# Performance work log

Hardware: AMD Instinct MI355X
Metric: run time of the kernel (lower is better)

Reference implementation:

```python
import jax, jax.numpy as jnp
import numpy as np

S, W, H = 1025, 128, 200


def setup_inputs() -> dict:
    key = jax.random.key(0)
    ks = jax.random.split(key, 40)
    n = lambda k, shape, s=1.0: jax.random.normal(k, shape, dtype=jnp.float32) * s
    p = {}
    p["words"] = n(ks[0], (S, W, H))
    p["lengths"] = jax.random.randint(ks[1], (S,), 1, W + 1, dtype=jnp.int32)
    p["h0w"] = n(ks[2], (S, H))
    p["c0w"] = n(ks[3], (S, H))
    p["h0p"] = n(ks[4], (H,))
    p["c0p"] = n(ks[5], (H,))
    p["h0q"] = n(ks[6], (H,))
    p["c0q"] = n(ks[7], (H,))
    ki = 8
    for nm in ("ctx", "tgt", "prev", "post"):
        p[f"wih_{nm}"] = n(ks[ki], (4 * H, H), 0.05); ki += 1
        p[f"whh_{nm}"] = n(ks[ki], (4 * H, H), 0.05); ki += 1
        p[f"bih_{nm}"] = n(ks[ki], (4 * H,), 0.05); ki += 1
        p[f"bhh_{nm}"] = n(ks[ki], (4 * H,), 0.05); ki += 1
    p["fc_w"] = n(ks[ki], (H, 2 * H), 0.05); ki += 1
    p["fc_b"] = n(ks[ki], (H,), 0.05)
    return p


def _lstm_seq(x, h0, c0, wih, whh, bih, bhh):
    """x: [T,H]; returns outputs [T,H]. Torch LSTM gate order: i,f,g,o."""
    gx = x @ wih.T + (bih + bhh)  # precompute input projection: [T,4H]
    def step(carry, g):
        h, c = carry
        gates = g + h @ whh.T
        i, f, gg, o = jnp.split(gates, 4, axis=-1)
        c = jax.nn.sigmoid(f) * c + jax.nn.sigmoid(i) * jnp.tanh(gg)
        h = jax.nn.sigmoid(o) * jnp.tanh(c)
        return (h, c), h
    _, hs = jax.lax.scan(step, (h0, c0), gx)
    return hs


def reference(words, lengths, h0w, c0w, h0p, c0p, h0q, c0q,
              wih_ctx, whh_ctx, bih_ctx, bhh_ctx,
              wih_tgt, whh_tgt, bih_tgt, bhh_tgt,
              wih_prev, whh_prev, bih_prev, bhh_prev,
              wih_post, whh_post, bih_post, bhh_post,
              fc_w, fc_b):
    Sn = words.shape[0]
    mid = (Sn - 1) // 2
    # Word-level context RNN over all sentences (batched scan)
    ctx_outs = jax.vmap(_lstm_seq, in_axes=(0, 0, 0, None, None, None, None))(
        words, h0w, c0w, wih_ctx, whh_ctx, bih_ctx, bhh_ctx)  # [S,W,H]
    # sentence embedding = output at last real word (ragged lengths)
    emb = ctx_outs[jnp.arange(Sn), lengths - 1]  # [S,H]
    # middle sentence uses target RNN instead
    tgt_outs = _lstm_seq(words[mid], h0w[mid], c0w[mid], wih_tgt, whh_tgt, bih_tgt, bhh_tgt)
    emb = emb.at[mid].set(tgt_outs[lengths[mid] - 1])
    # prev RNN over sentences 0..mid; keep output at mid
    prev_hs = _lstm_seq(emb[:mid + 1], h0p, c0p, wih_prev, whh_prev, bih_prev, bhh_prev)
    prev_out = prev_hs[-1]
    # post RNN over sentences S-1..mid (reversed); keep output at mid
    post_hs = _lstm_seq(emb[mid:][::-1], h0q, c0q, wih_post, whh_post, bih_post, bhh_post)
    post_out = post_hs[-1]
    feat = jnp.concatenate([prev_out, post_out])  # [2H]
    return feat @ fc_w.T + fc_b  # [H]
```

## Files before the change

### kernel.cpp

```cpp
#include <hip/hip_runtime.h>
#include <cmath>

typedef unsigned short u16;
typedef short bf16x8 __attribute__((ext_vector_type(8)));
typedef float f32x4 __attribute__((ext_vector_type(4)));

#define S_N 1025
#define W_N 128
#define H_N 200
#define FH_N 800
#define KP 232
#define SGP 911
#define SGW 900
#define MID 512
#define NT 56
#define PKT (NT * 7 * 512)

__device__ __forceinline__ float bf2f(u16 u) {
  unsigned int x = ((unsigned int)u) << 16;
  return __builtin_bit_cast(float, x);
}
__device__ __forceinline__ u16 f2bf(float f) {
  unsigned int x = __builtin_bit_cast(unsigned int, f);
  x += 0x7fffu + ((x >> 16) & 1u);
  return (u16)(x >> 16);
}
#define LOG2E 1.44269504088896f
__device__ __forceinline__ float fsigm(float x) {
  float e = __builtin_amdgcn_exp2f(-fabsf(x) * LOG2E);
  float p = __builtin_amdgcn_rcpf(1.f + e);
  return x >= 0.f ? p : 1.f - p;
}
__device__ __forceinline__ float ftanh(float x) {
  float e = __builtin_amdgcn_exp2f(-2.f * fabsf(x) * LOG2E);
  float th = (1.f - e) * __builtin_amdgcn_rcpf(1.f + e);
  return x >= 0.f ? th : -th;
}

__device__ __forceinline__ const bf16x8* pkptr(const u16* pk, int tt, int kcc, int lane) {
  return (const bf16x8*)(pk + (size_t)((tt * 7 + kcc) * 512 + lane * 8));
}

__device__ __forceinline__ int bfidx(int m, int k) {
  return (k >> 5) * 512 + ((((k >> 3) & 3) * 16 + m) << 3) + (k & 7);
}

__global__ __launch_bounds__(256) void k_w2b(
    const float* __restrict__ p0, const float* __restrict__ p1,
    const float* __restrict__ p2, const float* __restrict__ p3,
    const float* __restrict__ p4, const float* __restrict__ p5,
    const float* __restrict__ p6, const float* __restrict__ p7,
    u16* __restrict__ dst)
{
  int i = blockIdx.x * 256 + threadIdx.x;
  if (i >= 8 * PKT) return;
  int w = i / PKT, r = i - w * PKT;
  int tt = r / 3584;
  int q = r - tt * 3584;
  int kcc = q >> 9;
  int lane = (q >> 3) & 63;
  int j = q & 7;
  int col = lane & 15, quad = lane >> 4;
  int gate = tt * 16 + col;
  int k = kcc * 32 + quad * 8 + j;
  const float* ps[8] = {p0, p1, p2, p3, p4, p5, p6, p7};
  u16 v = 0;
  if (gate < FH_N && k < H_N) v = f2bf(ps[w][(size_t)gate * H_N + k]);
  dst[i] = v;
}

__global__ __launch_bounds__(1024) void k_sort(
    const int* __restrict__ lengths, int* __restrict__ order)
{
  __shared__ int key[2048], val[2048];
  int tid = threadIdx.x;
  for (int v = 0; v < 2; ++v) {
    int i = tid + v * 1024;
    key[i] = (i < S_N) ? lengths[i] : -1;
    val[i] = (i < S_N) ? i : (S_N - 1);
  }
  __syncthreads();
  for (int k = 2; k <= 2048; k <<= 1)
    for (int j = k >> 1; j > 0; j >>= 1) {
      for (int v = 0; v < 2; ++v) {
        int i = tid + v * 1024;
        int ix = i ^ j;
        if (ix > i) {
          bool descRegion = ((i & k) == 0);
          int ki = key[i], kx = key[ix];
          if ((ki < kx) == descRegion) {
            key[i] = kx; key[ix] = ki;
            int tv = val[i]; val[i] = val[ix]; val[ix] = tv;
          }
        }
      }
      __syncthreads();
    }
  for (int v = 0; v < 2; ++v) {
    int i = tid + v * 1024;
    if (i < S_N) order[i] = val[i];
  }
}

__global__ __launch_bounds__(512, 1) void k_xpack(
    int c, int CH,
    const float* __restrict__ words, const int* __restrict__ lengths,
    const u16* __restrict__ wihb_ctx, const float* __restrict__ bih_ctx, const float* __restrict__ bhh_ctx,
    const u16* __restrict__ wihb_tgt, const float* __restrict__ bih_tgt, const float* __restrict__ bhh_tgt,
    float* __restrict__ gxc)
{
  const int slot = blockIdx.x % 1026;
  const int tile = blockIdx.x / 1026;
  const int t0f = tile * 16;
  const bool tg = (slot == 1025);
  const int s = tg ? MID : slot;
  const int len = lengths[s];
  const int tbase = c * CH + t0f;
  if (t0f >= CH || tbase >= len) return;
  const u16* wih = tg ? wihb_tgt : wihb_ctx;
  const float* bih = tg ? bih_tgt : bih_ctx;
  const float* bhh = tg ? bhh_tgt : bhh_ctx;

  __shared__ __align__(16) u16 sXh[7 * 512];
  __shared__ __align__(16) u16 sXl[7 * 512];
  __shared__ float sBias[FH_N];
  const int tid = threadIdx.x;
  for (int e = tid; e < 7 * 512; e += 512) { sXh[e] = 0; sXl[e] = 0; }
  for (int e = tid; e < FH_N; e += 512) sBias[e] = bih[e] + bhh[e];
  __syncthreads();
  const int nrow = min(16, min(CH - t0f, len - tbase));
  for (int e = tid; e < nrow * H_N; e += 512) {
    int tr = e / H_N, k = e - tr * H_N;
    float v = words[((size_t)s * W_N + tbase + tr) * H_N + k];
    u16 vh = f2bf(v);
    int idx = bfidx(tr, k);
    sXh[idx] = vh;
    sXl[idx] = f2bf(v - bf2f(vh));
  }
  __syncthreads();

  const int lane = tid & 63, wv = tid >> 6, quad = lane >> 4, col = lane & 15;
  f32x4 acc[7];
#pragma unroll
  for (int i = 0; i < 7; ++i) { f32x4 z = {0.f, 0.f, 0.f, 0.f}; acc[i] = z; }

#pragma unroll
  for (int kcc = 0; kcc < 7; ++kcc) {
    bf16x8 Aw[7];
#pragma unroll
    for (int i = 0; i < 7; ++i) Aw[i] = *pkptr(wih, wv + 8 * i, kcc, lane);
    bf16x8 bxh = *(const bf16x8*)(sXh + kcc * 512 + lane * 8);
    bf16x8 bxl = *(const bf16x8*)(sXl + kcc * 512 + lane * 8);
#pragma unroll
    for (int i = 0; i < 7; ++i) {
      acc[i] = __builtin_amdgcn_mfma_f32_16x16x32_bf16(Aw[i], bxh, acc[i], 0, 0, 0);
      acc[i] = __builtin_amdgcn_mfma_f32_16x16x32_bf16(Aw[i], bxl, acc[i], 0, 0, 0);
    }
  }

  const int tcg = t0f + col;
  const bool okcol = (tcg < CH) && (c * CH + tcg < len);
#pragma unroll
  for (int i = 0; i < 7; ++i) {
    int tt = wv + 8 * i;
    if (tt < 50 && okcol) {
      float bias0 = sBias[tt * 16 + quad * 4 + 0];
      float bias1 = sBias[tt * 16 + quad * 4 + 1];
      float bias2 = sBias[tt * 16 + quad * 4 + 2];
      float bias3 = sBias[tt * 16 + quad * 4 + 3];
      f32x4 o = {acc[i][0] + bias0, acc[i][1] + bias1, acc[i][2] + bias2, acc[i][3] + bias3};
      *(f32x4*)(gxc + ((size_t)slot * CH + tcg) * FH_N + tt * 16 + quad * 4) = o;
    }
  }
}

__global__ __launch_bounds__(512, 1) void k_wrec(
    int c, int CH,
    const int* __restrict__ lengths, const int* __restrict__ order,
    const float* __restrict__ h0w, const float* __restrict__ c0w,
    const u16* __restrict__ whhb_ctx, const u16* __restrict__ whhb_tgt,
    const float* __restrict__ gxc,
    float* __restrict__ stateH, float* __restrict__ stateC,
    float* __restrict__ emb)
{
  const int tid = threadIdx.x;
  const int b = blockIdx.x;
  const bool is_tgt = (b == 65);
  const u16* whh = is_tgt ? whhb_tgt : whhb_ctx;

  __shared__ __align__(16) u16 sBh[7 * 512];
  __shared__ __align__(16) u16 sBl[7 * 512];
  __shared__ float sG[16 * SGW];
  __shared__ int sLen[16], sId[16];

  if (tid < 16) {
    int slot = b * 16 + tid;
    int s = is_tgt ? MID : order[min(slot, S_N - 1)];
    sId[tid] = s;
    sLen[tid] = lengths[s];
  }
  __syncthreads();
  int Lmax = 1;
  for (int m = 0; m < 16; ++m) Lmax = max(Lmax, sLen[m]);
  if (c * CH >= Lmax) return;

  const int lane = tid & 63;
  const int wv = tid >> 6;
  const int quad = lane >> 4;
  const int col = lane & 15;

  bf16x8 afr[7][7];
#pragma unroll
  for (int i = 0; i < 7; ++i)
#pragma unroll
    for (int kcc = 0; kcc < 7; ++kcc)
      afr[i][kcc] = *pkptr(whh, wv + 8 * i, kcc, lane);

  for (int e = tid; e < 7 * 512; e += 512) { sBh[e] = 0; sBl[e] = 0; }
  __syncthreads();

  float creg[7];
#pragma unroll
  for (int rr = 0; rr < 7; ++rr) {
    int e = tid + 512 * rr;
    if (e < 16 * H_N) {
      int m = e / H_N, j = e - m * H_N;
      float h, cc;
      if (c == 0) {
        int s = sId[m];
        h = h0w[(size_t)s * H_N + j];
        cc = c0w[(size_t)s * H_N + j];
      } else {
        h = stateH[(size_t)(b * 16 + m) * H_N + j];
        cc = stateC[(size_t)(b * 16 + m) * H_N + j];
      }
      creg[rr] = cc;
      u16 hh = f2bf(h);
      int idx = bfidx(m, j);
      sBh[idx] = hh;
      sBl[idx] = f2bf(h - bf2f(hh));
    }
  }
  __syncthreads();

#pragma unroll 1
  for (int tc = 0; tc < CH; ++tc) {
    const int t = c * CH + tc;
    if (t >= Lmax) break;

    f32x4 acc[7];
#pragma unroll
    for (int i = 0; i < 7; ++i) { f32x4 z = {0.f, 0.f, 0.f, 0.f}; acc[i] = z; }
#pragma unroll
    for (int kcc = 0; kcc < 7; ++kcc) {
      bf16x8 bh = *(const bf16x8*)(sBh + kcc * 512 + lane * 8);
      bf16x8 bl = *(const bf16x8*)(sBl + kcc * 512 + lane * 8);
#pragma unroll
      for (int i = 0; i < 7; ++i) {
        acc[i] = __builtin_amdgcn_mfma_f32_16x16x32_bf16(afr[i][kcc], bh, acc[i], 0, 0, 0);
        acc[i] = __builtin_amdgcn_mfma_f32_16x16x32_bf16(afr[i][kcc], bl, acc[i], 0, 0, 0);
      }
    }
#pragma unroll
    for (int i = 0; i < 7; ++i) {
      int tt = wv + 8 * i;
      *(f32x4*)(sG + col * SGW + tt * 16 + quad * 4) = acc[i];
    }
    __syncthreads();

#pragma unroll
    for (int rr = 0; rr < 7; ++rr) {
      int e = tid + 512 * rr;
      if (e < 16 * H_N) {
        int m = e / H_N, j = e - m * H_N;
        int gslot = is_tgt ? 1025 : sId[m];
        const float* gp = gxc + ((size_t)gslot * CH + tc) * FH_N + j;
        const float* gRow = sG + m * SGW + j;
        float ig = gRow[0] + gp[0];
        float fg = gRow[H_N] + gp[H_N];
        float gg = gRow[2 * H_N] + gp[2 * H_N];
        float og = gRow[3 * H_N] + gp[3 * H_N];
        float nc = fsigm(fg) * creg[rr] + fsigm(ig) * ftanh(gg);
        float nh = fsigm(og) * ftanh(nc);
        creg[rr] = nc;
        u16 hh = f2bf(nh);
        int idx = bfidx(m, j);
        sBh[idx] = hh;
        sBl[idx] = f2bf(nh - bf2f(hh));
        if (t == sLen[m] - 1) {
          int s = sId[m];
          if (is_tgt) {
            if (m == 0) emb[(size_t)MID * H_N + j] = nh;
          } else if (s != MID) {
            emb[(size_t)s * H_N + j] = nh;
          }
        }
      }
    }
    __syncthreads();
  }

#pragma unroll
  for (int rr = 0; rr < 7; ++rr) {
    int e = tid + 512 * rr;
    if (e < 16 * H_N) {
      int m = e / H_N, j = e - m * H_N;
      int idx = bfidx(m, j);
      stateH[(size_t)(b * 16 + m) * H_N + j] = bf2f(sBh[idx]) + bf2f(sBl[idx]);
      stateC[(size_t)(b * 16 + m) * H_N + j] = creg[rr];
    }
  }
}

__global__ __launch_bounds__(512, 1) void k_word_s(
    const float* __restrict__ words, const int* __restrict__ lengths,
    const int* __restrict__ order,
    const float* __restrict__ h0w, const float* __restrict__ c0w,
    const u16* __restrict__ wihb_ctx, const u16* __restrict__ whhb_ctx,
    const float* __restrict__ bih_ctx, const float* __restrict__ bhh_ctx,
    const u16* __restrict__ wihb_tgt, const u16* __restrict__ whhb_tgt,
    const float* __restrict__ bih_tgt, const float* __restrict__ bhh_tgt,
    float* __restrict__ emb)
{
  const int tid = threadIdx.x;
  const int b = blockIdx.x;
  const bool is_tgt = (b == 65);
  const u16* wih = is_tgt ? wihb_tgt : wihb_ctx;
  const u16* whh = is_tgt ? whhb_tgt : whhb_ctx;
  const float* bih = is_tgt ? bih_tgt : bih_ctx;
  const float* bhh = is_tgt ? bhh_tgt : bhh_ctx;

  __shared__ __align__(16) u16 sXhi[16 * KP];
  __shared__ __align__(16) u16 sXlo[16 * KP];
  __shared__ __align__(16) u16 sHi[16 * KP];
  __shared__ __align__(16) u16 sLo[16 * KP];
  __shared__ float sG[8 * SGP];
  __shared__ float sB[4 * H_N];
  __shared__ int sLen[16], sId[16];

  for (int e = tid; e < 16 * KP; e += 512) {
    sXhi[e] = 0; sXlo[e] = 0; sHi[e] = 0; sLo[e] = 0;
  }
  if (tid < 16) {
    int slot = b * 16 + tid;
    int s = is_tgt ? MID : order[min(slot, S_N - 1)];
    sId[tid] = s;
    sLen[tid] = lengths[s];
  }
  for (int e = tid; e < 4 * H_N; e += 512) sB[e] = bih[e] + bhh[e];
  __syncthreads();

  float creg[7];
#pragma unroll
  for (int r = 0; r < 7; ++r) {
    int e = tid + 512 * r;
    if (e < 16 * H_N) {
      int m = e / H_N, j = e - m * H_N;
      int s = sId[m];
      float h = h0w[(size_t)s * H_N + j];
      u16 hh = f2bf(h);
      sHi[m * KP + j] = hh;
      sLo[m * KP + j] = f2bf(h - bf2f(hh));
      creg[r] = c0w[(size_t)s * H_N + j];
    }
  }
  __syncthreads();
  int Lmax = 1;
  for (int m = 0; m < 16; ++m) Lmax = max(Lmax, sLen[m]);

  const int lane = tid & 63;
  const int wv = tid >> 6;
  const int quad = lane >> 4;
  const int col = lane & 15;
  const int hpass = quad >> 1;

  const u16* aXh = sXhi + col * KP + quad * 8;
  const u16* aXl = sXlo + col * KP + quad * 8;
  const u16* aHh = sHi  + col * KP + quad * 8;
  const u16* aHl = sLo  + col * KP + quad * 8;

#pragma unroll 1
  for (int t = 0; t < Lmax; ++t) {
    for (int e = tid; e < 16 * H_N; e += 512) {
      int m = e / H_N, k = e - m * H_N;
      float v = words[((size_t)sId[m] * W_N + t) * H_N + k];
      u16 vh = f2bf(v);
      sXhi[m * KP + k] = vh;
      sXlo[m * KP + k] = f2bf(v - bf2f(vh));
    }
    __syncthreads();

    f32x4 acc[7];
#pragma unroll
    for (int i = 0; i < 7; ++i) { f32x4 z4 = {0.f, 0.f, 0.f, 0.f}; acc[i] = z4; }

#pragma unroll
    for (int kcc = 0; kcc < 7; ++kcc) {
      bf16x8 axh = *(const bf16x8*)(aXh + kcc * 32);
      bf16x8 axl = *(const bf16x8*)(aXl + kcc * 32);
      bf16x8 ahh = *(const bf16x8*)(aHh + kcc * 32);
      bf16x8 ahl = *(const bf16x8*)(aHl + kcc * 32);
#pragma unroll
      for (int i = 0; i < 7; ++i) {
        bf16x8 bw = *pkptr(wih, wv + 8 * i, kcc, lane);
        bf16x8 bh = *pkptr(whh, wv + 8 * i, kcc, lane);
        acc[i] = __builtin_amdgcn_mfma_f32_16x16x32_bf16(axh, bw, acc[i], 0, 0, 0);
        acc[i] = __builtin_amdgcn_mfma_f32_16x16x32_bf16(axl, bw, acc[i], 0, 0, 0);
        acc[i] = __builtin_amdgcn_mfma_f32_16x16x32_bf16(ahh, bh, acc[i], 0, 0, 0);
        acc[i] = __builtin_amdgcn_mfma_f32_16x16x32_bf16(ahl, bh, acc[i], 0, 0, 0);
      }
    }

#pragma unroll 1
    for (int h = 0; h < 2; ++h) {
      if (hpass == h) {
#pragma unroll
        for (int i = 0; i < 7; ++i) {
          int tt = wv + 8 * i;
#pragma unroll
          for (int r = 0; r < 4; ++r)
            sG[((quad & 1) * 4 + r) * SGP + tt * 16 + col] = acc[i][r];
        }
      }
      __syncthreads();
#pragma unroll
      for (int rr = 0; rr < 7; ++rr) {
        int e = tid + 512 * rr;
        if (e < 16 * H_N) {
          int m = e / H_N, j = e - m * H_N;
          if ((m >> 3) == h) {
            const float* gRow = sG + (m - 8 * h) * SGP;
            float ig = gRow[j] + sB[j];
            float fg = gRow[H_N + j] + sB[H_N + j];
            float gg = gRow[2 * H_N + j] + sB[2 * H_N + j];
            float og = gRow[3 * H_N + j] + sB[3 * H_N + j];
            float nc = fsigm(fg) * creg[rr] + fsigm(ig) * ftanh(gg);
            float nh = fsigm(og) * ftanh(nc);
            creg[rr] = nc;
            u16 hh = f2bf(nh);
            sHi[m * KP + j] = hh;
            sLo[m * KP + j] = f2bf(nh - bf2f(hh));
            if (t == sLen[m] - 1) {
              int s = sId[m];
              if (is_tgt) {
                if (m == 0) emb[(size_t)MID * H_N + j] = nh;
              } else if (s != MID) {
                emb[(size_t)s * H_N + j] = nh;
              }
            }
          }
        }
      }
      __syncthreads();
    }
  }
}

__global__ __launch_bounds__(512) void k_gx(
    const float* __restrict__ emb,
    const u16* __restrict__ wihb_prev, const float* __restrict__ bih_prev, const float* __restrict__ bhh_prev,
    const u16* __restrict__ wihb_post, const float* __restrict__ bih_post, const float* __restrict__ bhh_post,
    float* __restrict__ gxp, float* __restrict__ gxq)
{
  const int tid = threadIdx.x;
  const int b = blockIdx.x;
  const bool post = (b >= 33);
  const int t0 = (post ? b - 33 : b) * 16;
  const u16* wih = post ? wihb_post : wihb_prev;
  const float* bih = post ? bih_post : bih_prev;
  const float* bhh = post ? bhh_post : bhh_prev;
  float* out = post ? gxq : gxp;

  __shared__ __align__(16) u16 sEhi[16 * KP];
  __shared__ __align__(16) u16 sElo[16 * KP];
  for (int e = tid; e < 16 * KP; e += 512) { sEhi[e] = 0; sElo[e] = 0; }
  __syncthreads();
  for (int e = tid; e < 16 * H_N; e += 512) {
    int m = e / H_N, k = e - m * H_N;
    int t = t0 + m;
    if (t <= 512) {
      int src = post ? (1024 - t) : t;
      float v = emb[(size_t)src * H_N + k];
      u16 vh = f2bf(v);
      sEhi[m * KP + k] = vh;
      sElo[m * KP + k] = f2bf(v - bf2f(vh));
    }
  }
  __syncthreads();

  const int lane = tid & 63;
  const int wv = tid >> 6;
  const int quad = lane >> 4;
  const int col = lane & 15;
  const u16* aH = sEhi + col * KP + quad * 8;
  const u16* aL = sElo + col * KP + quad * 8;

#pragma unroll 1
  for (int i = 0; i < 7; ++i) {
    int tt = wv + 8 * i;
    if (tt >= 50) break;
    int gate = tt * 16 + col;
    f32x4 acc = {0.f, 0.f, 0.f, 0.f};
#pragma unroll
    for (int kcc = 0; kcc < 7; ++kcc) {
      bf16x8 Ah = *(const bf16x8*)(aH + kcc * 32);
      bf16x8 Al = *(const bf16x8*)(aL + kcc * 32);
      bf16x8 bw = *pkptr(wih, tt, kcc, lane);
      acc = __builtin_amdgcn_mfma_f32_16x16x32_bf16(Ah, bw, acc, 0, 0, 0);
      acc = __builtin_amdgcn_mfma_f32_16x16x32_bf16(Al, bw, acc, 0, 0, 0);
    }
    float bias = bih[gate] + bhh[gate];
#pragma unroll
    for (int r = 0; r < 4; ++r) {
      int t = t0 + quad * 4 + r;
      if (t <= 512) out[(size_t)t * FH_N + gate] = acc[r] + bias;
    }
  }
}

__global__ __launch_bounds__(512, 1) void k_sent(
    const u16* __restrict__ whhb_prev, const u16* __restrict__ whhb_post,
    const float* __restrict__ h0p, const float* __restrict__ c0p,
    const float* __restrict__ h0q, const float* __restrict__ c0q,
    const float* __restrict__ gxp, const float* __restrict__ gxq,
    float* __restrict__ outp, float* __restrict__ outq)
{
  const int tid = threadIdx.x;
  const bool post = (blockIdx.x != 0);
  const u16* whh = post ? whhb_post : whhb_prev;
  const float* h0 = post ? h0q : h0p;
  const float* c0 = post ? c0q : c0p;
  const float* gx = post ? gxq : gxp;
  float* outv = post ? outq : outp;

  __shared__ __align__(16) u16 sHi[224];
  __shared__ __align__(16) u16 sLo[224];
  __shared__ float sGa[FH_N];
  __shared__ float sGb[FH_N];

  const int lane = tid & 63;
  const int wv = tid >> 6;
  const int quad = lane >> 4;
  const int col = lane & 15;

  bf16x8 afr[7][7];
#pragma unroll
  for (int i = 0; i < 7; ++i)
#pragma unroll
    for (int kcc = 0; kcc < 7; ++kcc)
      afr[i][kcc] = *pkptr(whh, wv + 8 * i, kcc, lane);

  if (tid < 224) { sHi[tid] = 0; sLo[tid] = 0; }
  float c = 0.f, last_h = 0.f;
  if (tid < H_N) {
    float h = h0[tid];
    u16 hh = f2bf(h);
    sHi[tid] = hh;
    sLo[tid] = f2bf(h - bf2f(hh));
    c = c0[tid];
  }
  __syncthreads();

  const u16* hb = ((lane & 8) ? sLo : sHi) + quad * 8;
  const bool wrA = (col == 0), wrB = (col == 8);

#pragma unroll 1
  for (int t = 0; t < 513; ++t) {
    bf16x8 bfr[7];
#pragma unroll
    for (int kcc = 0; kcc < 7; ++kcc) bfr[kcc] = *(const bf16x8*)(hb + kcc * 32);

#pragma unroll
    for (int i = 0; i < 7; ++i) {
      int tt = wv + 8 * i;
      f32x4 acc = {0.f, 0.f, 0.f, 0.f};
#pragma unroll
      for (int kcc = 0; kcc < 7; ++kcc)
        acc = __builtin_amdgcn_mfma_f32_16x16x32_bf16(afr[i][kcc], bfr[kcc], acc, 0, 0, 0);
      if (tt < 50) {
        if (wrA) {
#pragma unroll
          for (int r = 0; r < 4; ++r) sGa[tt * 16 + quad * 4 + r] = acc[r];
        } else if (wrB) {
#pragma unroll
          for (int r = 0; r < 4; ++r) sGb[tt * 16 + quad * 4 + r] = acc[r];
        }
      }
    }
    __syncthreads();

    if (tid < H_N) {
      const float* g = gx + (size_t)t * FH_N;
      float ig = sGa[tid] + sGb[tid] + g[tid];
      float fg = sGa[H_N + tid] + sGb[H_N + tid] + g[H_N + tid];
      float gg = sGa[2 * H_N + tid] + sGb[2 * H_N + tid] + g[2 * H_N + tid];
      float og = sGa[3 * H_N + tid] + sGb[3 * H_N + tid] + g[3 * H_N + tid];
      float nc = fsigm(fg) * c + fsigm(ig) * ftanh(gg);
      float nh = fsigm(og) * ftanh(nc);
      c = nc;
      last_h = nh;
      u16 hh = f2bf(nh);
      sHi[tid] = hh;
      sLo[tid] = f2bf(nh - bf2f(hh));
    }
    __syncthreads();
  }
  if (tid < H_N) outv[tid] = last_h;
}

__global__ __launch_bounds__(256) void k_fc(
    const float* __restrict__ pout, const float* __restrict__ qout,
    const float* __restrict__ fc_w, const float* __restrict__ fc_b,
    float* __restrict__ out)
{
  const int tid = threadIdx.x;
  if (tid < H_N) {
    float d = fc_b[tid];
    const float* wr = fc_w + (size_t)tid * 2 * H_N;
    for (int k = 0; k < H_N; ++k) d += pout[k] * wr[k];
    for (int k = 0; k < H_N; ++k) d += qout[k] * wr[H_N + k];
    out[tid] = d;
  }
}

extern "C" void kernel_launch(void* const* d_in, const int* in_sizes, int n_in,
                              void* d_out, int out_size, void* d_ws, size_t ws_size,
                              hipStream_t stream) {
  const float* words   = (const float*)d_in[0];
  const int*   lengths = (const int*)d_in[1];
  const float* h0w = (const float*)d_in[2];
  const float* c0w = (const float*)d_in[3];
  const float* h0p = (const float*)d_in[4];
  const float* c0p = (const float*)d_in[5];
  const float* h0q = (const float*)d_in[6];
  const float* c0q = (const float*)d_in[7];
  const float* wih_ctx = (const float*)d_in[8];
  const float* whh_ctx = (const float*)d_in[9];
  const float* bih_ctx = (const float*)d_in[10];
  const float* bhh_ctx = (const float*)d_in[11];
  const float* wih_tgt = (const float*)d_in[12];
  const float* whh_tgt = (const float*)d_in[13];
  const float* bih_tgt = (const float*)d_in[14];
  const float* bhh_tgt = (const float*)d_in[15];
  const float* wih_prev = (const float*)d_in[16];
  const float* whh_prev = (const float*)d_in[17];
  const float* bih_prev = (const float*)d_in[18];
  const float* bhh_prev = (const float*)d_in[19];
  const float* wih_post = (const float*)d_in[20];
  const float* whh_post = (const float*)d_in[21];
  const float* bih_post = (const float*)d_in[22];
  const float* bhh_post = (const float*)d_in[23];
  const float* fc_w = (const float*)d_in[24];
  const float* fc_b = (const float*)d_in[25];
  (void)in_sizes; (void)n_in; (void)out_size;

  const size_t FIXF = 1448600;
  int CH = 0;
  for (int cand = 32; cand >= 1; cand >>= 1) {
    size_t needB = ((size_t)1026 * cand * 800 + FIXF) * 4 + 1056 * 4 + (size_t)8 * PKT * 2 + 256;
    if (ws_size >= needB) { CH = cand; break; }
  }

  float* ws = (float*)d_ws;
  float *gxc, *stateH, *stateC, *emb, *gxp, *gxq, *po, *qo;
  int* order;
  u16* wb;
  if (CH > 0) {
    gxc = ws;
    stateH = gxc + (size_t)1026 * CH * 800;
    stateC = stateH + 211200;
    emb = stateC + 211200;
    gxp = emb + 205000;
    gxq = gxp + 410400;
    po = gxq + 410400;
    qo = po + 200;
    order = (int*)(qo + 200);
    wb = (u16*)(order + 1056);
  } else {
    gxc = nullptr; stateH = nullptr; stateC = nullptr;
    emb = ws;
    gxp = ws + 205000;
    gxq = ws + 615400;
    po = ws + 1025800;
    qo = ws + 1026000;
    order = (int*)(ws + 1026200);
    wb = (u16*)(ws + 1027232);
  }
  u16* wihb_ctx  = wb;
  u16* whhb_ctx  = wb + PKT;
  u16* wihb_tgt  = wb + 2 * PKT;
  u16* whhb_tgt  = wb + 3 * PKT;
  u16* whhb_prev = wb + 4 * PKT;
  u16* whhb_post = wb + 5 * PKT;
  u16* wihb_prev = wb + 6 * PKT;
  u16* wihb_post = wb + 7 * PKT;

  k_w2b<<<(8 * PKT + 255) / 256, 256, 0, stream>>>(
      wih_ctx, whh_ctx, wih_tgt, whh_tgt, whh_prev, whh_post,
      wih_prev, wih_post, wb);
  k_sort<<<1, 1024, 0, stream>>>(lengths, order);

  if (CH > 0) {
    const int TT = (CH + 15) / 16;
    const int NC = (W_N + CH - 1) / CH;
    for (int c = 0; c < NC; ++c) {
      k_xpack<<<1026 * TT, 512, 0, stream>>>(c, CH, words, lengths,
                                             wihb_ctx, bih_ctx, bhh_ctx,
                                             wihb_tgt, bih_tgt, bhh_tgt, gxc);
      k_wrec<<<66, 512, 0, stream>>>(c, CH, lengths, order, h0w, c0w,
                                     whhb_ctx, whhb_tgt, gxc, stateH, stateC, emb);
    }
  } else {
    k_word_s<<<66, 512, 0, stream>>>(words, lengths, order, h0w, c0w,
                                     wihb_ctx, whhb_ctx, bih_ctx, bhh_ctx,
                                     wihb_tgt, whhb_tgt, bih_tgt, bhh_tgt, emb);
  }
  k_gx<<<66, 512, 0, stream>>>(emb, wihb_prev, bih_prev, bhh_prev,
                               wihb_post, bih_post, bhh_post, gxp, gxq);
  k_sent<<<2, 512, 0, stream>>>(whhb_prev, whhb_post, h0p, c0p, h0q, c0q,
                                gxp, gxq, po, qo);
  k_fc<<<1, 256, 0, stream>>>(po, qo, fc_w, fc_b, (float*)d_out);
}
```

Before: 2.415 ms.

## Interleave gate rows so LSTM cell updates run from MFMA accumulators in registers

Permutes the packed weight rows and biases so each MFMA output quad holds the i,f,g,o gates of one hidden unit. The cell update can then run directly on accumulator registers with no shared-memory gate staging and one fewer barrier per step. It also double-buffers the hidden-state fragments with padded strides, has each k_xpack block handle two 16-step tiles to reuse the loaded weights, and prefetches the next step's input gates in the sentence recurrence. The risks are higher register pressure, and k_xpack now handles only two tiles, which assumes CH is at most 32.

```diff
diff --git a/kernel.cpp b/kernel.cpp
--- a/kernel.cpp
+++ b/kernel.cpp
@@ -11,10 +11,12 @@
 #define FH_N 800
 #define KP 232
 #define SGP 911
-#define SGW 900
 #define MID 512
 #define NT 56
 #define PKT (NT * 7 * 512)
+#define PKC 544
+#define QKS 136
+#define FRAGSZ (7 * PKC)
 
 __device__ __forceinline__ float bf2f(u16 u) {
   unsigned int x = ((unsigned int)u) << 16;
@@ -37,12 +39,16 @@
   return x >= 0.f ? th : -th;
 }
 
+__device__ __forceinline__ int gperm(int rp) { return (rp & 3) * H_N + (rp >> 2); }
+
 __device__ __forceinline__ const bf16x8* pkptr(const u16* pk, int tt, int kcc, int lane) {
   return (const bf16x8*)(pk + (size_t)((tt * 7 + kcc) * 512 + lane * 8));
 }
-
-__device__ __forceinline__ int bfidx(int m, int k) {
-  return (k >> 5) * 512 + ((((k >> 3) & 3) * 16 + m) << 3) + (k & 7);
+__device__ __forceinline__ int fidx(int m, int k) {
+  return (k >> 5) * PKC + ((k >> 3) & 3) * QKS + m * 8 + (k & 7);
+}
+__device__ __forceinline__ const bf16x8* frg(const u16* base, int kcc, int lane) {
+  return (const bf16x8*)(base + kcc * PKC + (lane >> 4) * QKS + (lane & 15) * 8);
 }
 
 __global__ __launch_bounds__(256) void k_w2b(
@@ -65,7 +71,7 @@
   int k = kcc * 32 + quad * 8 + j;
   const float* ps[8] = {p0, p1, p2, p3, p4, p5, p6, p7};
   u16 v = 0;
-  if (gate < FH_N && k < H_N) v = f2bf(ps[w][(size_t)gate * H_N + k]);
+  if (gate < FH_N && k < H_N) v = f2bf(ps[w][(size_t)gperm(gate) * H_N + k]);
   dst[i] = v;
 }
 
@@ -109,67 +115,86 @@
     const u16* __restrict__ wihb_tgt, const float* __restrict__ bih_tgt, const float* __restrict__ bhh_tgt,
     float* __restrict__ gxc)
 {
-  const int slot = blockIdx.x % 1026;
-  const int tile = blockIdx.x / 1026;
-  const int t0f = tile * 16;
+  const int slot = blockIdx.x;
   const bool tg = (slot == 1025);
   const int s = tg ? MID : slot;
   const int len = lengths[s];
-  const int tbase = c * CH + t0f;
-  if (t0f >= CH || tbase >= len) return;
+  const int tb0 = c * CH;
+  if (tb0 >= len) return;
   const u16* wih = tg ? wihb_tgt : wihb_ctx;
   const float* bih = tg ? bih_tgt : bih_ctx;
   const float* bhh = tg ? bhh_tgt : bhh_ctx;
 
-  __shared__ __align__(16) u16 sXh[7 * 512];
-  __shared__ __align__(16) u16 sXl[7 * 512];
+  __shared__ __align__(16) u16 sXh[2][FRAGSZ];
+  __shared__ __align__(16) u16 sXl[2][FRAGSZ];
   __shared__ float sBias[FH_N];
   const int tid = threadIdx.x;
-  for (int e = tid; e < 7 * 512; e += 512) { sXh[e] = 0; sXl[e] = 0; }
-  for (int e = tid; e < FH_N; e += 512) sBias[e] = bih[e] + bhh[e];
-  __syncthreads();
-  const int nrow = min(16, min(CH - t0f, len - tbase));
-  for (int e = tid; e < nrow * H_N; e += 512) {
-    int tr = e / H_N, k = e - tr * H_N;
-    float v = words[((size_t)s * W_N + tbase + tr) * H_N + k];
-    u16 vh = f2bf(v);
-    int idx = bfidx(tr, k);
-    sXh[idx] = vh;
-    sXl[idx] = f2bf(v - bf2f(vh));
+  for (int e = tid; e < FRAGSZ; e += 512) {
+    sXh[0][e] = 0; sXl[0][e] = 0; sXh[1][e] = 0; sXl[1][e] = 0;
+  }
+  for (int e = tid; e < FH_N; e += 512) sBias[e] = bih[gperm(e)] + bhh[gperm(e)];
+  __syncthreads();
+
+  const int nt = min(2, (min(CH, len - tb0) + 15) >> 4);
+  for (int jt = 0; jt < nt; ++jt) {
+    int nrow = min(16, min(CH - jt * 16, len - tb0 - jt * 16));
+    for (int e = tid; e < nrow * H_N; e += 512) {
+      int tr = e / H_N, k = e - tr * H_N;
+      float v = words[((size_t)s * W_N + tb0 + jt * 16 + tr) * H_N + k];
+      u16 vh = f2bf(v);
+      int idx = fidx(tr, k);
+      sXh[jt][idx] = vh;
+      sXl[jt][idx] = f2bf(v - bf2f(vh));
+    }
   }
   __syncthreads();
 
   const int lane = tid & 63, wv = tid >> 6, quad = lane >> 4, col = lane & 15;
-  f32x4 acc[7];
-#pragma unroll
-  for (int i = 0; i < 7; ++i) { f32x4 z = {0.f, 0.f, 0.f, 0.f}; acc[i] = z; }
+  f32x4 acc[2][7];
+#pragma unroll
+  for (int jt = 0; jt < 2; ++jt)
+#pragma unroll
+    for (int i = 0; i < 7; ++i) { f32x4 z = {0.f, 0.f, 0.f, 0.f}; acc[jt][i] = z; }
 
 #pragma unroll
   for (int kcc = 0; kcc < 7; ++kcc) {
     bf16x8 Aw[7];
 #pragma unroll
     for (int i = 0; i < 7; ++i) Aw[i] = *pkptr(wih, wv + 8 * i, kcc, lane);
-    bf16x8 bxh = *(const bf16x8*)(sXh + kcc * 512 + lane * 8);
-    bf16x8 bxl = *(const bf16x8*)(sXl + kcc * 512 + lane * 8);
-#pragma unroll
-    for (int i = 0; i < 7; ++i) {
-      acc[i] = __builtin_amdgcn_mfma_f32_16x16x32_bf16(Aw[i], bxh, acc[i], 0, 0, 0);
-      acc[i] = __builtin_amdgcn_mfma_f32_16x16x32_bf16(Aw[i], bxl, acc[i], 0, 0, 0);
-    }
-  }
-
-  const int tcg = t0f + col;
-  const bool okcol = (tcg < CH) && (c * CH + tcg < len);
-#pragma unroll
-  for (int i = 0; i < 7; ++i) {
-    int tt = wv + 8 * i;
-    if (tt < 50 && okcol) {
-      float bias0 = sBias[tt * 16 + quad * 4 + 0];
-      float bias1 = sBias[tt * 16 + quad * 4 + 1];
-      float bias2 = sBias[tt * 16 + quad * 4 + 2];
-      float bias3 = sBias[tt * 16 + quad * 4 + 3];
-      f32x4 o = {acc[i][0] + bias0, acc[i][1] + bias1, acc[i][2] + bias2, acc[i][3] + bias3};
-      *(f32x4*)(gxc + ((size_t)slot * CH + tcg) * FH_N + tt * 16 + quad * 4) = o;
+#pragma unroll
+    for (int jt = 0; jt < 2; ++jt) {
+      if (jt < nt) {
+        bf16x8 bxh = *frg(sXh[jt], kcc, lane);
+        bf16x8 bxl = *frg(sXl[jt], kcc, lane);
+#pragma unroll
+        for (int i = 0; i < 7; ++i) {
+          acc[jt][i] = __builtin_amdgcn_mfma_f32_16x16x32_bf16(Aw[i], bxh, acc[jt][i], 0, 0, 0);
+          acc[jt][i] = __builtin_amdgcn_mfma_f32_16x16x32_bf16(Aw[i], bxl, acc[jt][i], 0, 0, 0);
+        }
+      }
+    }
+  }
+
+#pragma unroll
+  for (int jt = 0; jt < 2; ++jt) {
+    if (jt < nt) {
+      int tcg = jt * 16 + col;
+      bool ok = (tcg < CH) && (tb0 + tcg < len);
+      if (ok) {
+#pragma unroll
+        for (int i = 0; i < 7; ++i) {
+          int tt = wv + 8 * i;
+          if (tt < 50) {
+            float b0 = sBias[tt * 16 + quad * 4 + 0];
+            float b1 = sBias[tt * 16 + quad * 4 + 1];
+            float b2 = sBias[tt * 16 + quad * 4 + 2];
+            float b3 = sBias[tt * 16 + quad * 4 + 3];
+            f32x4 o = {acc[jt][i][0] + b0, acc[jt][i][1] + b1,
+                       acc[jt][i][2] + b2, acc[jt][i][3] + b3};
+            *(f32x4*)(gxc + ((size_t)slot * CH + tcg) * FH_N + tt * 16 + quad * 4) = o;
+          }
+        }
+      }
     }
   }
 }
@@ -188,9 +213,8 @@
   const bool is_tgt = (b == 65);
   const u16* whh = is_tgt ? whhb_tgt : whhb_ctx;
 
-  __shared__ __align__(16) u16 sBh[7 * 512];
-  __shared__ __align__(16) u16 sBl[7 * 512];
-  __shared__ float sG[16 * SGW];
+  __shared__ __align__(16) u16 sBh[2][FRAGSZ];
+  __shared__ __align__(16) u16 sBl[2][FRAGSZ];
   __shared__ int sLen[16], sId[16];
 
   if (tid < 16) {
@@ -199,6 +223,9 @@
     sId[tid] = s;
     sLen[tid] = lengths[s];
   }
+  for (int e = tid; e < FRAGSZ; e += 512) {
+    sBh[0][e] = 0; sBl[0][e] = 0; sBh[1][e] = 0; sBl[1][e] = 0;
+  }
   __syncthreads();
   int Lmax = 1;
   for (int m = 0; m < 16; ++m) Lmax = max(Lmax, sLen[m]);
@@ -208,6 +235,8 @@
   const int wv = tid >> 6;
   const int quad = lane >> 4;
   const int col = lane & 15;
+  const int myS = sId[col];
+  const int myLen = sLen[col];
 
   bf16x8 afr[7][7];
 #pragma unroll
@@ -216,30 +245,23 @@
     for (int kcc = 0; kcc < 7; ++kcc)
       afr[i][kcc] = *pkptr(whh, wv + 8 * i, kcc, lane);
 
-  for (int e = tid; e < 7 * 512; e += 512) { sBh[e] = 0; sBl[e] = 0; }
-  __syncthreads();
-
-  float creg[7];
-#pragma unroll
-  for (int rr = 0; rr < 7; ++rr) {
-    int e = tid + 512 * rr;
-    if (e < 16 * H_N) {
-      int m = e / H_N, j = e - m * H_N;
-      float h, cc;
+  float creg[7], hreg[7];
+#pragma unroll
+  for (int i = 0; i < 7; ++i) {
+    int uu = 4 * (wv + 8 * i) + quad;
+    if (uu < H_N) {
       if (c == 0) {
-        int s = sId[m];
-        h = h0w[(size_t)s * H_N + j];
-        cc = c0w[(size_t)s * H_N + j];
+        hreg[i] = h0w[(size_t)myS * H_N + uu];
+        creg[i] = c0w[(size_t)myS * H_N + uu];
       } else {
-        h = stateH[(size_t)(b * 16 + m) * H_N + j];
-        cc = stateC[(size_t)(b * 16 + m) * H_N + j];
-      }
-      creg[rr] = cc;
-      u16 hh = f2bf(h);
-      int idx = bfidx(m, j);
-      sBh[idx] = hh;
-      sBl[idx] = f2bf(h - bf2f(hh));
-    }
+        hreg[i] = stateH[(size_t)(b * 16 + col) * H_N + uu];
+        creg[i] = stateC[(size_t)(b * 16 + col) * H_N + uu];
+      }
+      u16 hh = f2bf(hreg[i]);
+      int idx = fidx(col, uu);
+      sBh[0][idx] = hh;
+      sBl[0][idx] = f2bf(hreg[i] - bf2f(hh));
+    } else { creg[i] = 0.f; hreg[i] = 0.f; }
   }
   __syncthreads();
 
@@ -247,52 +269,52 @@
   for (int tc = 0; tc < CH; ++tc) {
     const int t = c * CH + tc;
     if (t >= Lmax) break;
+    const int cb = tc & 1, nb = cb ^ 1;
+    const int gslot = is_tgt ? 1025 : myS;
+    const float* gbase = gxc + ((size_t)gslot * CH + tc) * FH_N;
+
+    f32x4 gv[7];
+#pragma unroll
+    for (int i = 0; i < 7; ++i) {
+      int uu = 4 * (wv + 8 * i) + quad;
+      if (uu < H_N) gv[i] = *(const f32x4*)(gbase + 4 * uu);
+    }
 
     f32x4 acc[7];
 #pragma unroll
     for (int i = 0; i < 7; ++i) { f32x4 z = {0.f, 0.f, 0.f, 0.f}; acc[i] = z; }
 #pragma unroll
     for (int kcc = 0; kcc < 7; ++kcc) {
-      bf16x8 bh = *(const bf16x8*)(sBh + kcc * 512 + lane * 8);
-      bf16x8 bl = *(const bf16x8*)(sBl + kcc * 512 + lane * 8);
+      bf16x8 bh = *frg(sBh[cb], kcc, lane);
+      bf16x8 bl = *frg(sBl[cb], kcc, lane);
 #pragma unroll
       for (int i = 0; i < 7; ++i) {
         acc[i] = __builtin_amdgcn_mfma_f32_16x16x32_bf16(afr[i][kcc], bh, acc[i], 0, 0, 0);
         acc[i] = __builtin_amdgcn_mfma_f32_16x16x32_bf16(afr[i][kcc], bl, acc[i], 0, 0, 0);
       }
     }
+
 #pragma unroll
     for (int i = 0; i < 7; ++i) {
-      int tt = wv + 8 * i;
-      *(f32x4*)(sG + col * SGW + tt * 16 + quad * 4) = acc[i];
-    }
-    __syncthreads();
-
-#pragma unroll
-    for (int rr = 0; rr < 7; ++rr) {
-      int e = tid + 512 * rr;
-      if (e < 16 * H_N) {
-        int m = e / H_N, j = e - m * H_N;
-        int gslot = is_tgt ? 1025 : sId[m];
-        const float* gp = gxc + ((size_t)gslot * CH + tc) * FH_N + j;
-        const float* gRow = sG + m * SGW + j;
-        float ig = gRow[0] + gp[0];
-        float fg = gRow[H_N] + gp[H_N];
-        float gg = gRow[2 * H_N] + gp[2 * H_N];
-        float og = gRow[3 * H_N] + gp[3 * H_N];
-        float nc = fsigm(fg) * creg[rr] + fsigm(ig) * ftanh(gg);
+      int uu = 4 * (wv + 8 * i) + quad;
+      if (uu < H_N) {
+        float ig = acc[i][0] + gv[i][0];
+        float fg = acc[i][1] + gv[i][1];
+        float gg = acc[i][2] + gv[i][2];
+        float og = acc[i][3] + gv[i][3];
+        float nc = fsigm(fg) * creg[i] + fsigm(ig) * ftanh(gg);
         float nh = fsigm(og) * ftanh(nc);
-        creg[rr] = nc;
+        creg[i] = nc;
+        hreg[i] = nh;
         u16 hh = f2bf(nh);
-        int idx = bfidx(m, j);
-        sBh[idx] = hh;
-        sBl[idx] = f2bf(nh - bf2f(hh));
-        if (t == sLen[m] - 1) {
-          int s = sId[m];
+        int idx = fidx(col, uu);
+        sBh[nb][idx] = hh;
+        sBl[nb][idx] = f2bf(nh - bf2f(hh));
+        if (t == myLen - 1) {
           if (is_tgt) {
-            if (m == 0) emb[(size_t)MID * H_N + j] = nh;
-          } else if (s != MID) {
-            emb[(size_t)s * H_N + j] = nh;
+            if (col == 0) emb[(size_t)MID * H_N + uu] = nh;
+          } else if (myS != MID) {
+            emb[(size_t)myS * H_N + uu] = nh;
           }
         }
       }
@@ -301,13 +323,11 @@
   }
 
 #pragma unroll
-  for (int rr = 0; rr < 7; ++rr) {
-    int e = tid + 512 * rr;
-    if (e < 16 * H_N) {
-      int m = e / H_N, j = e - m * H_N;
-      int idx = bfidx(m, j);
-      stateH[(size_t)(b * 16 + m) * H_N + j] = bf2f(sBh[idx]) + bf2f(sBl[idx]);
-      stateC[(size_t)(b * 16 + m) * H_N + j] = creg[rr];
+  for (int i = 0; i < 7; ++i) {
+    int uu = 4 * (wv + 8 * i) + quad;
+    if (uu < H_N) {
+      stateH[(size_t)(b * 16 + col) * H_N + uu] = hreg[i];
+      stateC[(size_t)(b * 16 + col) * H_N + uu] = creg[i];
     }
   }
 }
@@ -347,7 +367,7 @@
     sId[tid] = s;
     sLen[tid] = lengths[s];
   }
-  for (int e = tid; e < 4 * H_N; e += 512) sB[e] = bih[e] + bhh[e];
+  for (int e = tid; e < 4 * H_N; e += 512) sB[e] = bih[gperm(e)] + bhh[gperm(e)];
   __syncthreads();
 
   float creg[7];
@@ -429,11 +449,11 @@
         if (e < 16 * H_N) {
           int m = e / H_N, j = e - m * H_N;
           if ((m >> 3) == h) {
-            const float* gRow = sG + (m - 8 * h) * SGP;
-            float ig = gRow[j] + sB[j];
-            float fg = gRow[H_N + j] + sB[H_N + j];
-            float gg = gRow[2 * H_N + j] + sB[2 * H_N + j];
-            float og = gRow[3 * H_N + j] + sB[3 * H_N + j];
+            const float* gRow = sG + (m - 8 * h) * SGP + 4 * j;
+            float ig = gRow[0] + sB[4 * j + 0];
+            float fg = gRow[1] + sB[4 * j + 1];
+            float gg = gRow[2] + sB[4 * j + 2];
+            float og = gRow[3] + sB[4 * j + 3];
             float nc = fsigm(fg) * creg[rr] + fsigm(ig) * ftanh(gg);
             float nh = fsigm(og) * ftanh(nc);
             creg[rr] = nc;
@@ -509,7 +529,7 @@
       acc = __builtin_amdgcn_mfma_f32_16x16x32_bf16(Ah, bw, acc, 0, 0, 0);
       acc = __builtin_amdgcn_mfma_f32_16x16x32_bf16(Al, bw, acc, 0, 0, 0);
     }
-    float bias = bih[gate] + bhh[gate];
+    float bias = bih[gperm(gate)] + bhh[gperm(gate)];
 #pragma unroll
     for (int r = 0; r < 4; ++r) {
       int t = t0 + quad * 4 + r;
@@ -533,10 +553,8 @@
   const float* gx = post ? gxq : gxp;
   float* outv = post ? outq : outp;
 
-  __shared__ __align__(16) u16 sHi[224];
-  __shared__ __align__(16) u16 sLo[224];
-  __shared__ float sGa[FH_N];
-  __shared__ float sGb[FH_N];
+  __shared__ __align__(16) u16 sHi[2][224];
+  __shared__ __align__(16) u16 sLo[2][224];
 
   const int lane = tid & 63;
   const int wv = tid >> 6;
@@ -550,62 +568,69 @@
     for (int kcc = 0; kcc < 7; ++kcc)
       afr[i][kcc] = *pkptr(whh, wv + 8 * i, kcc, lane);
 
-  if (tid < 224) { sHi[tid] = 0; sLo[tid] = 0; }
-  float c = 0.f, last_h = 0.f;
+  if (tid < 224) { sHi[0][tid] = 0; sLo[0][tid] = 0; sHi[1][tid] = 0; sLo[1][tid] = 0; }
   if (tid < H_N) {
     float h = h0[tid];
     u16 hh = f2bf(h);
-    sHi[tid] = hh;
-    sLo[tid] = f2bf(h - bf2f(hh));
-    c = c0[tid];
-  }
-  __syncthreads();
-
-  const u16* hb = ((lane & 8) ? sLo : sHi) + quad * 8;
-  const bool wrA = (col == 0), wrB = (col == 8);
+    sHi[0][tid] = hh;
+    sLo[0][tid] = f2bf(h - bf2f(hh));
+  }
+
+  const int utile = wv + 8 * col;
+  const bool upd = (col < 7) && (utile < 50);
+  const int uu = 4 * utile + quad;
+  float c = upd ? c0[uu] : 0.f;
+  float last_h = 0.f;
+  f32x4 gcur = {0.f, 0.f, 0.f, 0.f};
+  if (upd) gcur = *(const f32x4*)(gx + 4 * uu);
+  __syncthreads();
 
 #pragma unroll 1
   for (int t = 0; t < 513; ++t) {
+    const int cb = t & 1, nb = cb ^ 1;
+    const u16* hb = ((lane & 8) ? sLo[cb] : sHi[cb]) + quad * 8;
     bf16x8 bfr[7];
 #pragma unroll
     for (int kcc = 0; kcc < 7; ++kcc) bfr[kcc] = *(const bf16x8*)(hb + kcc * 32);
 
+    f32x4 gnext = {0.f, 0.f, 0.f, 0.f};
+    if (t + 1 < 513 && upd) gnext = *(const f32x4*)(gx + (size_t)(t + 1) * FH_N + 4 * uu);
+
+    f32x4 acc[7];
+#pragma unroll
+    for (int i = 0; i < 7; ++i) { f32x4 z = {0.f, 0.f, 0.f, 0.f}; acc[i] = z; }
+#pragma unroll
+    for (int kcc = 0; kcc < 7; ++kcc)
+#pragma unroll
+      for (int i = 0; i < 7; ++i)
+        acc[i] = __builtin_amdgcn_mfma_f32_16x16x32_bf16(afr[i][kcc], bfr[kcc], acc[i], 0, 0, 0);
+
+    f32x4 gsel = {0.f, 0.f, 0.f, 0.f};
 #pragma unroll
     for (int i = 0; i < 7; ++i) {
-      int tt = wv + 8 * i;
-      f32x4 acc = {0.f, 0.f, 0.f, 0.f};
-#pragma unroll
-      for (int kcc = 0; kcc < 7; ++kcc)
-        acc = __builtin_amdgcn_mfma_f32_16x16x32_bf16(afr[i][kcc], bfr[kcc], acc, 0, 0, 0);
-      if (tt < 50) {
-        if (wrA) {
-#pragma unroll
-          for (int r = 0; r < 4; ++r) sGa[tt * 16 + quad * 4 + r] = acc[r];
-        } else if (wrB) {
-#pragma unroll
-          for (int r = 0; r < 4; ++r) sGb[tt * 16 + quad * 4 + r] = acc[r];
-        }
-      }
-    }
-    __syncthreads();
-
-    if (tid < H_N) {
-      const float* g = gx + (size_t)t * FH_N;
-      float ig = sGa[tid] + sGb[tid] + g[tid];
-      float fg = sGa[H_N + tid] + sGb[H_N + tid] + g[H_N + tid];
-      float gg = sGa[2 * H_N + tid] + sGb[2 * H_N + tid] + g[2 * H_N + tid];
-      float og = sGa[3 * H_N + tid] + sGb[3 * H_N + tid] + g[3 * H_N + tid];
+      f32x4 w;
+#pragma unroll
+      for (int r = 0; r < 4; ++r) w[r] = acc[i][r] + __shfl_xor(acc[i][r], 8);
+      if (col == i) gsel = w;
+    }
+
+    if (upd) {
+      float ig = gsel[0] + gcur[0];
+      float fg = gsel[1] + gcur[1];
+      float gg = gsel[2] + gcur[2];
+      float og = gsel[3] + gcur[3];
       float nc = fsigm(fg) * c + fsigm(ig) * ftanh(gg);
       float nh = fsigm(og) * ftanh(nc);
       c = nc;
       last_h = nh;
       u16 hh = f2bf(nh);
-      sHi[tid] = hh;
-      sLo[tid] = f2bf(nh - bf2f(hh));
-    }
+      sHi[nb][uu] = hh;
+      sLo[nb][uu] = f2bf(nh - bf2f(hh));
+    }
+    gcur = gnext;
     __syncthreads();
   }
-  if (tid < H_N) outv[tid] = last_h;
+  if (upd) outv[uu] = last_h;
 }
 
 __global__ __launch_bounds__(256) void k_fc(
@@ -701,12 +726,11 @@
   k_sort<<<1, 1024, 0, stream>>>(lengths, order);
 
   if (CH > 0) {
-    const int TT = (CH + 15) / 16;
     const int NC = (W_N + CH - 1) / CH;
     for (int c = 0; c < NC; ++c) {
-      k_xpack<<<1026 * TT, 512, 0, stream>>>(c, CH, words, lengths,
-                                             wihb_ctx, bih_ctx, bhh_ctx,
-                                             wihb_tgt, bih_tgt, bhh_tgt, gxc);
+      k_xpack<<<1026, 512, 0, stream>>>(c, CH, words, lengths,
+                                        wihb_ctx, bih_ctx, bhh_ctx,
+                                        wihb_tgt, bih_tgt, bhh_tgt, gxc);
       k_wrec<<<66, 512, 0, stream>>>(c, CH, lengths, order, h0w, c0w,
                                      whhb_ctx, whhb_tgt, gxc, stateH, stateC, emb);
     }
```

Result: no change. 2.446 ms (+1.3%).
